# Optimization experiments

Measured on AMD Instinct MI355X. Metric: run time of the kernel, lower is better.

Reference implementation:

```python
import jax, jax.numpy as jnp
import numpy as np

B, S, HID = 1, 2048, 4096
H, HKV, D = 32, 8, 128
GROUPS = H // HKV
ROPE_BASE = 10000.0


def setup_inputs() -> dict:
    key = jax.random.key(0)
    k1, k2, k3, k4, k5 = jax.random.split(key, 5)
    s = 0.02
    return {
        "hidden_states": jax.random.normal(k1, (B, S, HID), dtype=jnp.float32),
        "Wq": jax.random.normal(k2, (H * D, HID), dtype=jnp.float32) * s,
        "Wk": jax.random.normal(k3, (HKV * D, HID), dtype=jnp.float32) * s,
        "Wv": jax.random.normal(k4, (HKV * D, HID), dtype=jnp.float32) * s,
        "Wo": jax.random.normal(k5, (HID, H * D), dtype=jnp.float32) * s,
    }


def _rotate_half(x):
    x1, x2 = x[..., : D // 2], x[..., D // 2 :]
    return jnp.concatenate((-x2, x1), axis=-1)


def _rope_tables(seq_len):
    inv_freq = 1.0 / (ROPE_BASE ** (jnp.arange(0, D, 2, dtype=jnp.float32) / D))
    t = jnp.arange(seq_len, dtype=jnp.float32)
    freqs = jnp.outer(t, inv_freq)            # [S, D/2]
    emb = jnp.concatenate((freqs, freqs), -1)  # [S, D]
    return jnp.cos(emb)[None, None], jnp.sin(emb)[None, None]  # [1,1,S,D]


def reference(hidden_states, Wq, Wk, Wv, Wo):
    b, s, _ = hidden_states.shape
    scale = D ** -0.5
    q = (hidden_states @ Wq.T).reshape(b, s, H, D).transpose(0, 2, 1, 3)    # [B,H,S,D]
    k = (hidden_states @ Wk.T).reshape(b, s, HKV, D).transpose(0, 2, 1, 3)  # [B,HKV,S,D]
    v = (hidden_states @ Wv.T).reshape(b, s, HKV, D).transpose(0, 2, 1, 3)

    cos, sin = _rope_tables(s)
    q = q * cos + _rotate_half(q) * sin
    k = k * cos + _rotate_half(k) * sin

    # repeat_kv: h = kv_h * groups + g -> consecutive repeat along head axis
    k_rep = jnp.repeat(k, GROUPS, axis=1)  # [B,H,S,D]
    v_rep = jnp.repeat(v, GROUPS, axis=1)

    scores = jnp.einsum("bhqd,bhkd->bhqk", q, k_rep) * scale
    causal = jnp.tril(jnp.ones((s, s), dtype=bool))
    scores = jnp.where(causal[None, None], scores, jnp.finfo(scores.dtype).min)
    probs = jax.nn.softmax(scores, axis=-1)
    attn = jnp.einsum("bhqk,bhkd->bhqd", probs, v_rep)  # [B,H,S,D]
    attn = attn.transpose(0, 2, 1, 3).reshape(b, s, H * D)
    return attn @ Wo.T
```

## Files before the change

kernel.cpp:

```cpp
#include <hip/hip_runtime.h>

#define AS1 __attribute__((address_space(1)))
#define AS3 __attribute__((address_space(3)))

typedef __bf16 bf16;
typedef __bf16 bf16x8 __attribute__((ext_vector_type(8)));
typedef float f32x4 __attribute__((ext_vector_type(4)));

__device__ __forceinline__ void gld_lds16(const bf16* g, bf16* l) {
    __builtin_amdgcn_global_load_lds((const AS1 void*)g, (AS3 void*)l, 16, 0, 0);
}

#define SB0 __builtin_amdgcn_sched_barrier(0)
#define BARX do { SB0; __builtin_amdgcn_s_barrier(); SB0; } while (0)

__global__ void cvt4_kernel(const float4* __restrict__ in, ushort4* __restrict__ out, int n4) {
    const int i = blockIdx.x * 256 + threadIdx.x;
    if (i >= n4) return;
    const float4 v = in[i];
    ushort4 r;
    r.x = __builtin_bit_cast(unsigned short, (bf16)v.x);
    r.y = __builtin_bit_cast(unsigned short, (bf16)v.y);
    r.z = __builtin_bit_cast(unsigned short, (bf16)v.z);
    r.w = __builtin_bit_cast(unsigned short, (bf16)v.w);
    out[i] = r;
}

template <bool OUTF32>
__launch_bounds__(512, 2)
__global__ void gemm_8ph_kernel(const bf16* __restrict__ A, const bf16* __restrict__ W,
                                void* __restrict__ Cout, int M, int N, int K) {
    __shared__ __align__(16) bf16 Asl[2][256 * 64];
    __shared__ __align__(16) bf16 Bsl[2][256 * 64];

    const int tn = blockIdx.x * 256;
    const int tm = blockIdx.y * 256;
    const int tid = threadIdx.x;
    const int wave = tid >> 6;
    const int lane = tid & 63;
    const int laneR = lane & 15;
    const int laneS = lane >> 4;
    const int wmB = (wave >> 2) * 128;
    const int wnB = (wave & 3) * 64;
    const int NT = K >> 6;
    const int NI = NT >> 1;

    auto stageA = [&](int t, int h) {
        if (t >= NT) return;
        const int d = t & 1, k0 = t << 6;
#pragma unroll
        for (int iss = 0; iss < 2; ++iss) {
            const int c = iss * 512 + tid;
            const int row = c >> 3, sl = c & 7;
            gld_lds16(A + (size_t)(tm + h * 128 + row) * K + k0 + ((sl ^ (row & 7)) << 3),
                      &Asl[d][h * 8192 + (iss * 512 + wave * 64) * 8]);
        }
    };
    auto stageB = [&](int t, int h) {
        if (t >= NT) return;
        const int d = t & 1, k0 = t << 6;
#pragma unroll
        for (int iss = 0; iss < 2; ++iss) {
            const int c = iss * 512 + tid;
            const int row = c >> 3, sl = c & 7;
            gld_lds16(W + (size_t)(tn + h * 128 + row) * K + k0 + ((sl ^ (row & 7)) << 3),
                      &Bsl[d][h * 8192 + (iss * 512 + wave * 64) * 8]);
        }
    };

    bf16x8 aF[8], bF0[4], bF1[4];
    f32x4 acc[8][4] = {};

#define RD_A(d, mh) do { _Pragma("unroll") for (int m = 0; m < 4; ++m) \
    _Pragma("unroll") for (int ks = 0; ks < 2; ++ks) { \
        const int row_ = wmB + (mh) * 64 + m * 16 + laneR; \
        const int sl_ = (ks * 4 + laneS) ^ (row_ & 7); \
        aF[m * 2 + ks] = *(const bf16x8*)&Asl[d][row_ * 64 + sl_ * 8]; } } while (0)

#define RD_B(d, nh, DST) do { _Pragma("unroll") for (int n = 0; n < 2; ++n) \
    _Pragma("unroll") for (int ks = 0; ks < 2; ++ks) { \
        const int row_ = wnB + (nh) * 32 + n * 16 + laneR; \
        const int sl_ = (ks * 4 + laneS) ^ (row_ & 7); \
        DST[n * 2 + ks] = *(const bf16x8*)&Bsl[d][row_ * 64 + sl_ * 8]; } } while (0)

#define MMAQ(mh, nh, BSRC) do { __builtin_amdgcn_s_setprio(1); \
    _Pragma("unroll") for (int m = 0; m < 4; ++m) \
    _Pragma("unroll") for (int n = 0; n < 2; ++n) \
    _Pragma("unroll") for (int ks = 0; ks < 2; ++ks) \
        acc[(mh) * 4 + m][(nh) * 2 + n] = __builtin_amdgcn_mfma_f32_16x16x32_bf16( \
            aF[m * 2 + ks], BSRC[n * 2 + ks], acc[(mh) * 4 + m][(nh) * 2 + n], 0, 0, 0); \
    __builtin_amdgcn_s_setprio(0); } while (0)

    stageA(0, 0); stageA(0, 1); stageB(0, 0); stageB(0, 1); stageA(1, 0);
    SB0; asm volatile("s_waitcnt vmcnt(2)" ::: "memory"); BARX;

    for (int i = 0; i < NI; ++i) {
        const int u = i * 2;
        const bool last = (i == NI - 1);
        RD_A(0, 0); RD_B(0, 0, bF0); stageA(u + 1, 1);
        BARX; MMAQ(0, 0, bF0); BARX;
        RD_B(0, 1, bF1); stageB(u + 1, 0);
        BARX; MMAQ(0, 1, bF1); BARX;
        RD_A(0, 1); stageB(u + 1, 1);
        BARX; MMAQ(1, 1, bF1); BARX;
        RD_B(0, 0, bF0); stageA(u + 2, 0);
        BARX; MMAQ(1, 0, bF0);
        SB0;
        if (last) asm volatile("s_waitcnt vmcnt(0)" ::: "memory");
        else      asm volatile("s_waitcnt vmcnt(2)" ::: "memory");
        BARX;
        RD_A(1, 0); RD_B(1, 0, bF0); stageA(u + 2, 1);
        BARX; MMAQ(0, 0, bF0); BARX;
        RD_B(1, 1, bF1); stageB(u + 2, 0);
        BARX; MMAQ(0, 1, bF1); BARX;
        RD_A(1, 1); stageB(u + 2, 1);
        BARX; MMAQ(1, 1, bF1); BARX;
        RD_B(1, 0, bF0); stageA(u + 3, 0);
        BARX; MMAQ(1, 0, bF0);
        SB0;
        if (last) asm volatile("s_waitcnt vmcnt(0)" ::: "memory");
        else      asm volatile("s_waitcnt vmcnt(2)" ::: "memory");
        BARX;
    }
#undef RD_A
#undef RD_B
#undef MMAQ

    const int rbase = laneS * 4;
#pragma unroll
    for (int mf = 0; mf < 8; ++mf)
#pragma unroll
        for (int nf = 0; nf < 4; ++nf)
#pragma unroll
            for (int rr = 0; rr < 4; ++rr) {
                const size_t row = (size_t)tm + wmB + mf * 16 + rbase + rr;
                const size_t col = (size_t)tn + wnB + nf * 16 + laneR;
                if constexpr (OUTF32) ((float*)Cout)[row * N + col] = acc[mf][nf][rr];
                else                  ((bf16*)Cout)[row * N + col] = (bf16)acc[mf][nf][rr];
            }
    (void)M;
}

template <int BN, bool OUTF32>
__launch_bounds__(512, 2)
__global__ void gemm8p_kernel(const bf16* __restrict__ A, const bf16* __restrict__ W,
                              void* __restrict__ Cout, int M, int N, int K) {
    constexpr int NF = BN / 64;
    constexpr int IB = BN / 128;
    __shared__ __align__(16) bf16 Asl[4][128 * 32];
    __shared__ __align__(16) bf16 Bsl[4][BN * 32];

    const int tn = blockIdx.x * BN;
    const int tm = blockIdx.y * 128;
    const int tid = threadIdx.x;
    const int wave = tid >> 6;
    const int lane = tid & 63;
    const int laneR = lane & 15;
    const int laneS = lane >> 4;
    const int wmB = (wave >> 2) * 64;
    const int wnB = (wave & 3) * (BN / 4);
    const int NT = K >> 5;

    auto stage = [&](int t) {
        const int slot = t & 3;
        const int k0 = t << 5;
        {
            const int row = tid >> 2, g = tid & 3;
            gld_lds16(A + (size_t)(tm + row) * K + k0 + g * 8, &Asl[slot][wave * 512]);
        }
#pragma unroll
        for (int i = 0; i < IB; ++i) {
            const int row = i * 128 + (tid >> 2), g = tid & 3;
            gld_lds16(W + (size_t)(tn + row) * K + k0 + g * 8,
                      &Bsl[slot][i * 4096 + wave * 512]);
        }
    };

    f32x4 acc[4][NF] = {};

    stage(0); stage(1); stage(2);
    asm volatile("s_waitcnt vmcnt(6)" ::: "memory");
    SB0;
    __builtin_amdgcn_s_barrier();
    SB0;

    for (int t = 0; t < NT; ++t) {
        const int slot = t & 3;
        bf16x8 af[4], bfr[NF];
#pragma unroll
        for (int mf = 0; mf < 4; ++mf)
            af[mf] = *(const bf16x8*)&Asl[slot][(wmB + mf * 16 + laneR) * 32 + laneS * 8];
#pragma unroll
        for (int nf = 0; nf < NF; ++nf)
            bfr[nf] = *(const bf16x8*)&Bsl[slot][(wnB + nf * 16 + laneR) * 32 + laneS * 8];

        if (t + 3 < NT) stage(t + 3);

#pragma unroll
        for (int mf = 0; mf < 4; ++mf)
#pragma unroll
            for (int nf = 0; nf < NF; ++nf)
                acc[mf][nf] = __builtin_amdgcn_mfma_f32_16x16x32_bf16(af[mf], bfr[nf], acc[mf][nf], 0, 0, 0);

        SB0;
        if (t + 3 < NT)      asm volatile("s_waitcnt vmcnt(6)" ::: "memory");
        else if (t + 3 == NT) asm volatile("s_waitcnt vmcnt(3)" ::: "memory");
        else                  asm volatile("s_waitcnt vmcnt(0)" ::: "memory");
        SB0;
        __builtin_amdgcn_s_barrier();
        SB0;
    }

    const int rbase = laneS * 4;
#pragma unroll
    for (int mf = 0; mf < 4; ++mf)
#pragma unroll
        for (int nf = 0; nf < NF; ++nf)
#pragma unroll
            for (int rr = 0; rr < 4; ++rr) {
                const size_t row = (size_t)tm + wmB + mf * 16 + rbase + rr;
                const size_t col = (size_t)tn + wnB + nf * 16 + laneR;
                if constexpr (OUTF32) ((float*)Cout)[row * N + col] = acc[mf][nf][rr];
                else                  ((bf16*)Cout)[row * N + col] = (bf16)acc[mf][nf][rr];
            }
    (void)M;
}

__global__ void rope_qk_kernel(const bf16* __restrict__ C, bf16* __restrict__ Qr, bf16* __restrict__ Kr) {
    const int idx = blockIdx.x * 256 + threadIdx.x;
    const int NQ = 2048 * 32 * 64;
    const float QSC = 0.12751743561884394f;
    const float LN1E4_64 = 0.14391156831212787f;
    if (idx < NQ) {
        const int f = idx & 63;
        const int t = idx >> 6;
        const int h = t & 31;
        const int s = t >> 5;
        const float x1 = (float)C[(size_t)s * 6144 + h * 128 + f];
        const float x2 = (float)C[(size_t)s * 6144 + h * 128 + f + 64];
        const float th = s * expf(-LN1E4_64 * (float)f);
        const float cs = cosf(th), sn = sinf(th);
        bf16* dst = Qr + ((size_t)h * 2048 + s) * 128 + f;
        dst[0]  = (bf16)((x1 * cs - x2 * sn) * QSC);
        dst[64] = (bf16)((x2 * cs + x1 * sn) * QSC);
    } else {
        const int i2 = idx - NQ;
        const int f = i2 & 63;
        const int t = i2 >> 6;
        const int h = t & 7;
        const int s = t >> 3;
        const float x1 = (float)C[(size_t)s * 6144 + 4096 + h * 128 + f];
        const float x2 = (float)C[(size_t)s * 6144 + 4096 + h * 128 + f + 64];
        const float th = s * expf(-LN1E4_64 * (float)f);
        const float cs = cosf(th), sn = sinf(th);
        bf16* dst = Kr + ((size_t)h * 2048 + s) * 128 + f;
        dst[0]  = (bf16)(x1 * cs - x2 * sn);
        dst[64] = (bf16)(x2 * cs + x1 * sn);
    }
}

__global__ void transpose_v_kernel(const bf16* __restrict__ C, bf16* __restrict__ Vt) {
    __shared__ __align__(16) unsigned short t[64][136];
    const int hkv = blockIdx.x >> 5;
    const int st = blockIdx.x & 31;
    const int s0 = st * 64;
    const int tid = threadIdx.x;
#pragma unroll
    for (int it = 0; it < 4; ++it) {
        const int l = it * 2048 + tid * 8;
        const int r = l >> 7, c = l & 127;
        *(bf16x8*)&t[r][c] = *(const bf16x8*)&C[(size_t)(s0 + r) * 6144 + 5120 + hkv * 128 + c];
    }
    __syncthreads();
#pragma unroll
    for (int it = 0; it < 8; ++it) {
        const int o = it * 1024 + tid * 4;
        const int d = o >> 6, j = o & 63;
        ushort4 pk;
        pk.x = t[j + 0][d];
        pk.y = t[j + 1][d];
        pk.z = t[j + 2][d];
        pk.w = t[j + 3][d];
        *(ushort4*)&Vt[((size_t)hkv * 128 + d) * 2048 + s0 + j] = pk;
    }
}

__launch_bounds__(256, 1)
__global__ void flash_attn_kernel(const bf16* __restrict__ Qr, const bf16* __restrict__ Kr,
                                  const bf16* __restrict__ Vt, bf16* __restrict__ Aout) {
    __shared__ __align__(16) bf16 Klds[2][128 * 128];
    __shared__ __align__(16) bf16 Vlds[2][128 * 128];
    __shared__ __align__(16) char Plds[4][4096];

    const int bid = blockIdx.x;
    const int hkv = bid & 7;
    const int r = bid >> 3;
    const int h = hkv * 4 + (r & 3);
    const int pa = r >> 2;
    const int qbA = 15 - pa, qbB = pa;
    const int tid = threadIdx.x;
    const int wave = tid >> 6, lane = tid & 63;
    const int laneR = lane & 15;
    const int laneS = lane >> 4;
    const int laneK = laneS * 8;
    const int rbase = laneS * 4;

    const bf16* Kh = Kr + (size_t)hkv * 2048 * 128;
    const bf16* Vh = Vt + (size_t)hkv * 128 * 2048;
    char* Pw = Plds[wave];

    auto stageK = [&](int kv0, int buf) {
#pragma unroll
        for (int s = 0; s < 8; ++s) {
            const int chunk = wave * 8 + s;
            const int L = chunk * 64 + lane;
            const int row = L >> 4, sl = L & 15;
            gld_lds16(Kh + (size_t)(kv0 + row) * 128 + ((sl ^ (row & 7)) << 3),
                      &Klds[buf][chunk * 512]);
        }
    };
    auto stageV = [&](int kv0, int buf) {
#pragma unroll
        for (int s = 0; s < 8; ++s) {
            const int chunk = wave * 8 + s;
            const int L = chunk * 64 + lane;
            const int row = L >> 4, sl = L & 15;
            gld_lds16(Vh + (size_t)row * 2048 + kv0 + ((sl ^ (row & 7)) << 3),
                      &Vlds[buf][chunk * 512]);
        }
    };

    int qbcur = qbA;
    int q0w = qbA * 128 + wave * 32;
    int tloc = 0;

    bf16x8 qf[2][4];
    auto loadQ = [&]() {
#pragma unroll
        for (int mi = 0; mi < 2; ++mi)
#pragma unroll
            for (int kc = 0; kc < 4; ++kc)
                qf[mi][kc] = *(const bf16x8*)&Qr[((size_t)h * 2048 + q0w + mi * 16 + laneR) * 128 + kc * 32 + laneK];
    };
    loadQ();

    f32x4 o[2][8] = {};
    float mrow[2][4], lrow[2][4];
#pragma unroll
    for (int mi = 0; mi < 2; ++mi)
#pragma unroll
        for (int rr = 0; rr < 4; ++rr) { mrow[mi][rr] = -1e30f; lrow[mi][rr] = 0.f; }

    stageK(0, 0);
    stageV(0, 0);
    __syncthreads();

    for (int g = 0; g < 17; ++g) {
        const int buf = g & 1;
        if (g < 16) {
            const int tn = (g + 1 <= qbA) ? (g + 1) : (g - qbA);
            stageK(tn * 128, buf ^ 1);
            stageV(tn * 128, buf ^ 1);
        }
        const int kv0 = tloc * 128;

        f32x4 sc[2][8] = {};
        __builtin_amdgcn_s_setprio(1);
#pragma unroll
        for (int kc = 0; kc < 4; ++kc) {
            bf16x8 kf[8];
#pragma unroll
            for (int j = 0; j < 8; ++j) {
                const int row = j * 16 + laneR;
                kf[j] = *(const bf16x8*)((const char*)Klds[buf] + row * 256 +
                                         ((kc * 64 + laneS * 16) ^ ((row & 7) << 4)));
            }
#pragma unroll
            for (int mi = 0; mi < 2; ++mi)
#pragma unroll
                for (int j = 0; j < 8; ++j)
                    sc[mi][j] = __builtin_amdgcn_mfma_f32_16x16x32_bf16(qf[mi][kc], kf[j], sc[mi][j], 0, 0, 0);
        }
        __builtin_amdgcn_s_setprio(0);

        if (tloc == qbcur) {
#pragma unroll
            for (int mi = 0; mi < 2; ++mi)
#pragma unroll
                for (int j = 0; j < 8; ++j)
#pragma unroll
                    for (int rr = 0; rr < 4; ++rr) {
                        const int qr = q0w + mi * 16 + rbase + rr;
                        const int kr = kv0 + j * 16 + laneR;
                        if (kr > qr) sc[mi][j][rr] = -1e30f;
                    }
        }

#pragma unroll
        for (int mi = 0; mi < 2; ++mi) {
#pragma unroll
            for (int rr = 0; rr < 4; ++rr) {
                float v = sc[mi][0][rr];
#pragma unroll
                for (int j = 1; j < 8; ++j) v = fmaxf(v, sc[mi][j][rr]);
                v = fmaxf(v, __shfl_xor(v, 1, 64));
                v = fmaxf(v, __shfl_xor(v, 2, 64));
                v = fmaxf(v, __shfl_xor(v, 4, 64));
                v = fmaxf(v, __shfl_xor(v, 8, 64));
                float m0 = mrow[mi][rr];
                if (v - m0 > 8.0f) {
                    const float fac = __builtin_exp2f(m0 - v);
                    mrow[mi][rr] = v;
                    m0 = v;
                    lrow[mi][rr] *= fac;
#pragma unroll
                    for (int j = 0; j < 8; ++j) o[mi][j][rr] *= fac;
                }
                float rs = 0.f;
#pragma unroll
                for (int j = 0; j < 8; ++j) {
                    const float p = __builtin_exp2f(sc[mi][j][rr] - m0);
                    sc[mi][j][rr] = p;
                    rs += p;
                }
                rs += __shfl_xor(rs, 1, 64);
                rs += __shfl_xor(rs, 2, 64);
                rs += __shfl_xor(rs, 4, 64);
                rs += __shfl_xor(rs, 8, 64);
                lrow[mi][rr] += rs;
            }
        }

#pragma unroll
        for (int hf = 0; hf < 2; ++hf) {
#pragma unroll
            for (int mi = 0; mi < 2; ++mi)
#pragma unroll
                for (int j = 0; j < 4; ++j)
#pragma unroll
                    for (int rr = 0; rr < 4; ++rr) {
                        const int row = mi * 16 + rbase + rr;
                        *(bf16*)(Pw + row * 128 + ((j * 32 + laneR * 2) ^ ((row & 7) << 4))) =
                            (bf16)sc[mi][hf * 4 + j][rr];
                    }
            __builtin_amdgcn_s_setprio(1);
#pragma unroll
            for (int kc = 0; kc < 2; ++kc) {
                bf16x8 pf[2];
#pragma unroll
                for (int mi = 0; mi < 2; ++mi) {
                    const int row = mi * 16 + laneR;
                    pf[mi] = *(const bf16x8*)(Pw + row * 128 + ((kc * 64 + laneS * 16) ^ ((row & 7) << 4)));
                }
                const int kcg = hf * 2 + kc;
                bf16x8 vf[8];
#pragma unroll
                for (int j = 0; j < 8; ++j) {
                    const int row = j * 16 + laneR;
                    vf[j] = *(const bf16x8*)((const char*)Vlds[buf] + row * 256 +
                                             ((kcg * 64 + laneS * 16) ^ ((row & 7) << 4)));
                }
#pragma unroll
                for (int mi = 0; mi < 2; ++mi)
#pragma unroll
                    for (int j = 0; j < 8; ++j)
                        o[mi][j] = __builtin_amdgcn_mfma_f32_16x16x32_bf16(pf[mi], vf[j], o[mi][j], 0, 0, 0);
            }
            __builtin_amdgcn_s_setprio(0);
        }

        if (tloc == qbcur) {
#pragma unroll
            for (int mi = 0; mi < 2; ++mi) {
                float rinv[4];
#pragma unroll
                for (int rr = 0; rr < 4; ++rr) rinv[rr] = 1.0f / lrow[mi][rr];
#pragma unroll
                for (int j = 0; j < 8; ++j)
#pragma unroll
                    for (int rr = 0; rr < 4; ++rr) {
                        const size_t row = (size_t)q0w + mi * 16 + rbase + rr;
                        Aout[row * 4096 + h * 128 + j * 16 + laneR] = (bf16)(o[mi][j][rr] * rinv[rr]);
                    }
            }
            if (g < 16) {
                qbcur = qbB;
                q0w = qbB * 128 + wave * 32;
                tloc = 0;
                loadQ();
#pragma unroll
                for (int mi = 0; mi < 2; ++mi)
#pragma unroll
                    for (int rr = 0; rr < 4; ++rr) { mrow[mi][rr] = -1e30f; lrow[mi][rr] = 0.f; }
#pragma unroll
                for (int mi = 0; mi < 2; ++mi)
#pragma unroll
                    for (int j = 0; j < 8; ++j)
                        o[mi][j] = f32x4{0.f, 0.f, 0.f, 0.f};
            }
        } else {
            ++tloc;
        }

        __syncthreads();
    }
}

extern "C" void kernel_launch(void* const* d_in, const int* in_sizes, int n_in,
                              void* d_out, int out_size, void* d_ws, size_t ws_size,
                              hipStream_t stream) {
    const float* hidden = (const float*)d_in[0];
    const float* Wq = (const float*)d_in[1];
    const float* Wk = (const float*)d_in[2];
    const float* Wv = (const float*)d_in[3];
    const float* Wo = (const float*)d_in[4];
    float* out = (float*)d_out;
    char* ws = (char*)d_ws;

    bf16* hs = (bf16*)(ws + 0);
    bf16* Wb = (bf16*)(ws + 16777216);
    bf16* Cq = (bf16*)(ws + 100663296);
    bf16* Qr = (bf16*)(ws + 125829120);
    bf16* Kr = (bf16*)(ws + 142606336);
    bf16* Vt = (bf16*)(ws + 146800640);
    bf16* At = (bf16*)(ws + 150994944);
    (void)ws_size; (void)in_sizes; (void)n_in; (void)out_size;

    cvt4_kernel<<<8192, 256, 0, stream>>>((const float4*)hidden, (ushort4*)hs, 2097152);
    cvt4_kernel<<<16384, 256, 0, stream>>>((const float4*)Wq, (ushort4*)(Wb + 0), 4194304);
    cvt4_kernel<<<4096, 256, 0, stream>>>((const float4*)Wk, (ushort4*)(Wb + 16777216), 1048576);
    cvt4_kernel<<<4096, 256, 0, stream>>>((const float4*)Wv, (ushort4*)(Wb + 20971520), 1048576);
    cvt4_kernel<<<16384, 256, 0, stream>>>((const float4*)Wo, (ushort4*)(Wb + 25165824), 4194304);

    gemm_8ph_kernel<false><<<dim3(24, 8), 512, 0, stream>>>(hs, Wb, Cq, 2048, 6144, 4096);

    rope_qk_kernel<<<20480, 256, 0, stream>>>(Cq, Qr, Kr);

    transpose_v_kernel<<<256, 256, 0, stream>>>(Cq, Vt);

    flash_attn_kernel<<<256, 256, 0, stream>>>(Qr, Kr, Vt, At);

    gemm8p_kernel<256, true><<<dim3(16, 16), 512, 0, stream>>>(At, Wb + 25165824, out, 2048, 4096, 4096);
}
```

Measured before the change: 363.1 us.

## Swizzle LDS in output GEMM, fuse conversions, precompute RoPE tables

Applies an XOR swizzle to the 16-byte chunk placement in the output projection GEMM's LDS tiles, matching the global-load source offset and the fragment read offset, to reduce LDS bank conflicts. Merges the five fp32-to-bf16 conversion launches into a single kernel to cut launch overhead. Precomputes RoPE cos/sin tables once instead of recomputing transcendentals per element, storing them in workspace that aliases the already-consumed bf16 hidden-state buffer.

```diff
diff --git a/kernel.cpp b/kernel.cpp
--- a/kernel.cpp
+++ b/kernel.cpp
@@ -14,16 +14,25 @@
 #define SB0 __builtin_amdgcn_sched_barrier(0)
 #define BARX do { SB0; __builtin_amdgcn_s_barrier(); SB0; } while (0)
 
-__global__ void cvt4_kernel(const float4* __restrict__ in, ushort4* __restrict__ out, int n4) {
+__global__ void cvt_all_kernel(const float4* __restrict__ h, const float4* __restrict__ wq,
+                               const float4* __restrict__ wk, const float4* __restrict__ wv,
+                               const float4* __restrict__ wo, ushort4* __restrict__ hs,
+                               ushort4* __restrict__ wb) {
     const int i = blockIdx.x * 256 + threadIdx.x;
-    if (i >= n4) return;
-    const float4 v = in[i];
+    const float4* src;
+    ushort4* dst;
+    if (i < 2097152)      { src = h  + i;             dst = hs + i; }
+    else if (i < 6291456) { src = wq + (i - 2097152); dst = wb + (i - 2097152); }
+    else if (i < 7340032) { src = wk + (i - 6291456); dst = wb + 4194304 + (i - 6291456); }
+    else if (i < 8388608) { src = wv + (i - 7340032); dst = wb + 5242880 + (i - 7340032); }
+    else                  { src = wo + (i - 8388608); dst = wb + 6291456 + (i - 8388608); }
+    const float4 v = *src;
     ushort4 r;
     r.x = __builtin_bit_cast(unsigned short, (bf16)v.x);
     r.y = __builtin_bit_cast(unsigned short, (bf16)v.y);
     r.z = __builtin_bit_cast(unsigned short, (bf16)v.z);
     r.w = __builtin_bit_cast(unsigned short, (bf16)v.w);
-    out[i] = r;
+    *dst = r;
 }
 
 template <bool OUTF32>
@@ -160,18 +169,21 @@
     const int wmB = (wave >> 2) * 64;
     const int wnB = (wave & 3) * (BN / 4);
     const int NT = K >> 5;
+    const int sofs = (laneS ^ ((laneR >> 1) & 3)) << 3;
 
     auto stage = [&](int t) {
         const int slot = t & 3;
         const int k0 = t << 5;
         {
             const int row = tid >> 2, g = tid & 3;
-            gld_lds16(A + (size_t)(tm + row) * K + k0 + g * 8, &Asl[slot][wave * 512]);
+            const int sg = g ^ ((row >> 1) & 3);
+            gld_lds16(A + (size_t)(tm + row) * K + k0 + sg * 8, &Asl[slot][wave * 512]);
         }
 #pragma unroll
         for (int i = 0; i < IB; ++i) {
             const int row = i * 128 + (tid >> 2), g = tid & 3;
-            gld_lds16(W + (size_t)(tn + row) * K + k0 + g * 8,
+            const int sg = g ^ ((row >> 1) & 3);
+            gld_lds16(W + (size_t)(tn + row) * K + k0 + sg * 8,
                       &Bsl[slot][i * 4096 + wave * 512]);
         }
     };
@@ -189,10 +201,10 @@
         bf16x8 af[4], bfr[NF];
 #pragma unroll
         for (int mf = 0; mf < 4; ++mf)
-            af[mf] = *(const bf16x8*)&Asl[slot][(wmB + mf * 16 + laneR) * 32 + laneS * 8];
+            af[mf] = *(const bf16x8*)&Asl[slot][(wmB + mf * 16 + laneR) * 32 + sofs];
 #pragma unroll
         for (int nf = 0; nf < NF; ++nf)
-            bfr[nf] = *(const bf16x8*)&Bsl[slot][(wnB + nf * 16 + laneR) * 32 + laneS * 8];
+            bfr[nf] = *(const bf16x8*)&Bsl[slot][(wnB + nf * 16 + laneR) * 32 + sofs];
 
         if (t + 3 < NT) stage(t + 3);
 
@@ -203,7 +215,7 @@
                 acc[mf][nf] = __builtin_amdgcn_mfma_f32_16x16x32_bf16(af[mf], bfr[nf], acc[mf][nf], 0, 0, 0);
 
         SB0;
-        if (t + 3 < NT)      asm volatile("s_waitcnt vmcnt(6)" ::: "memory");
+        if (t + 3 < NT)       asm volatile("s_waitcnt vmcnt(6)" ::: "memory");
         else if (t + 3 == NT) asm volatile("s_waitcnt vmcnt(3)" ::: "memory");
         else                  asm volatile("s_waitcnt vmcnt(0)" ::: "memory");
         SB0;
@@ -226,11 +238,20 @@
     (void)M;
 }
 
-__global__ void rope_qk_kernel(const bf16* __restrict__ C, bf16* __restrict__ Qr, bf16* __restrict__ Kr) {
+__global__ void rope_table_kernel(float* __restrict__ ct, float* __restrict__ st) {
+    const int idx = blockIdx.x * 256 + threadIdx.x;
+    const int f = idx & 63;
+    const int s = idx >> 6;
+    const float th = s * expf(-0.14391156831212787f * (float)f);
+    ct[idx] = cosf(th);
+    st[idx] = sinf(th);
+}
+
+__global__ void rope_qk_kernel(const bf16* __restrict__ C, bf16* __restrict__ Qr, bf16* __restrict__ Kr,
+                               const float* __restrict__ ct, const float* __restrict__ st) {
     const int idx = blockIdx.x * 256 + threadIdx.x;
     const int NQ = 2048 * 32 * 64;
     const float QSC = 0.12751743561884394f;
-    const float LN1E4_64 = 0.14391156831212787f;
     if (idx < NQ) {
         const int f = idx & 63;
         const int t = idx >> 6;
@@ -238,8 +259,7 @@
         const int s = t >> 5;
         const float x1 = (float)C[(size_t)s * 6144 + h * 128 + f];
         const float x2 = (float)C[(size_t)s * 6144 + h * 128 + f + 64];
-        const float th = s * expf(-LN1E4_64 * (float)f);
-        const float cs = cosf(th), sn = sinf(th);
+        const float cs = ct[(s << 6) + f], sn = st[(s << 6) + f];
         bf16* dst = Qr + ((size_t)h * 2048 + s) * 128 + f;
         dst[0]  = (bf16)((x1 * cs - x2 * sn) * QSC);
         dst[64] = (bf16)((x2 * cs + x1 * sn) * QSC);
@@ -251,8 +271,7 @@
         const int s = t >> 3;
         const float x1 = (float)C[(size_t)s * 6144 + 4096 + h * 128 + f];
         const float x2 = (float)C[(size_t)s * 6144 + 4096 + h * 128 + f + 64];
-        const float th = s * expf(-LN1E4_64 * (float)f);
-        const float cs = cosf(th), sn = sinf(th);
+        const float cs = ct[(s << 6) + f], sn = st[(s << 6) + f];
         bf16* dst = Kr + ((size_t)h * 2048 + s) * 128 + f;
         dst[0]  = (bf16)(x1 * cs - x2 * sn);
         dst[64] = (bf16)(x2 * cs + x1 * sn);
@@ -524,17 +543,19 @@
     bf16* Kr = (bf16*)(ws + 142606336);
     bf16* Vt = (bf16*)(ws + 146800640);
     bf16* At = (bf16*)(ws + 150994944);
+    float* ct = (float*)(ws + 0);
+    float* st = (float*)(ws + 524288);
     (void)ws_size; (void)in_sizes; (void)n_in; (void)out_size;
 
-    cvt4_kernel<<<8192, 256, 0, stream>>>((const float4*)hidden, (ushort4*)hs, 2097152);
-    cvt4_kernel<<<16384, 256, 0, stream>>>((const float4*)Wq, (ushort4*)(Wb + 0), 4194304);
-    cvt4_kernel<<<4096, 256, 0, stream>>>((const float4*)Wk, (ushort4*)(Wb + 16777216), 1048576);
-    cvt4_kernel<<<4096, 256, 0, stream>>>((const float4*)Wv, (ushort4*)(Wb + 20971520), 1048576);
-    cvt4_kernel<<<16384, 256, 0, stream>>>((const float4*)Wo, (ushort4*)(Wb + 25165824), 4194304);
+    cvt_all_kernel<<<49152, 256, 0, stream>>>((const float4*)hidden, (const float4*)Wq,
+                                              (const float4*)Wk, (const float4*)Wv,
+                                              (const float4*)Wo, (ushort4*)hs, (ushort4*)Wb);
 
     gemm_8ph_kernel<false><<<dim3(24, 8), 512, 0, stream>>>(hs, Wb, Cq, 2048, 6144, 4096);
 
-    rope_qk_kernel<<<20480, 256, 0, stream>>>(Cq, Qr, Kr);
+    rope_table_kernel<<<512, 256, 0, stream>>>(ct, st);
+
+    rope_qk_kernel<<<20480, 256, 0, stream>>>(Cq, Qr, Kr, ct, st);
 
     transpose_v_kernel<<<256, 256, 0, stream>>>(Cq, Vt);
 
```

After: 351.1 us. 1.03x faster.
